# Kernel tuning notes

Measured on AMD Instinct MI355X. Metric: run time of the kernel, lower is better.

## Reference

```python
import jax, jax.numpy as jnp
import numpy as np

N, E, D_IN, D_OUT = 50000, 800000, 32, 64


def setup_inputs() -> dict:
    key = jax.random.key(0)
    k1, k2, k3 = jax.random.split(key, 3)
    x = jax.random.normal(k1, (N, D_IN), dtype=jnp.float32)
    edge_index = jax.random.randint(k2, (2, E), 0, N)
    W = jax.random.normal(k3, (D_IN, D_OUT), dtype=jnp.float32) / np.sqrt(D_IN).astype(np.float32)
    b = jnp.zeros((D_OUT,), dtype=jnp.float32)
    return {"x": x, "edge_index": edge_index, "W": W, "b": b}


def gcn_conv(x, edge_index, W, b):
    n = x.shape[0]
    loop = jnp.arange(n)
    src = jnp.concatenate([edge_index[0], loop])  # message sources (x_j)
    dst = jnp.concatenate([edge_index[1], loop])  # aggregation targets
    xw = x @ W  # [N, D_OUT]
    deg = jax.ops.segment_sum(jnp.ones(src.shape[0], dtype=xw.dtype), dst, num_segments=n)
    dinv = jnp.where(deg > 0, jax.lax.rsqrt(jnp.where(deg > 0, deg, 1.0)), 0.0)
    norm = dinv[src] * dinv[dst]  # [E+N]
    msg = xw[src] * norm[:, None]  # gather + scale
    out = jax.ops.segment_sum(msg, dst, num_segments=n)  # scatter-add aggregate
    return out + b


def reference(x, edge_index, W, b):
    h = jax.nn.relu(gcn_conv(x, edge_index, W, b))
    # InnerProductDecoder over given edges: sigmoid(<h_i, h_j>)
    logits = jnp.sum(h[edge_index[0]] * h[edge_index[1]], axis=-1)  # [E]
    adj_pred = jax.nn.sigmoid(logits) + 1e-15
    return (adj_pred, edge_index)
```

## Files before the change

### kernel.cpp

```cpp
#include <hip/hip_runtime.h>
#include <hip/hip_fp8.h>

#define D_IN 32
#define D_OUT 64
#define NBMAX 800
#define BIN_BLKS 128
#define COPY_BLKS 784
#define CAP 32
#define BCAP 1280

__device__ __forceinline__ unsigned char f2fp8(float f) {
    __hip_fp8_e4m3 v(f);
    return (unsigned char)v.__x;
}
__device__ __forceinline__ float fp82f(unsigned char u) {
    __hip_fp8_e4m3 v;
    v.__x = (__hip_fp8_storage_t)u;
    return (float)v;
}
__device__ __forceinline__ float bf2f(unsigned short u) {
    return __uint_as_float(((unsigned int)u) << 16);
}
__device__ __forceinline__ unsigned short f2bf(float f) {
    unsigned int x = __float_as_uint(f);
    x += 0x7fff + ((x >> 16) & 1);
    return (unsigned short)(x >> 16);
}
__device__ __forceinline__ float dot4fp8(unsigned int ua, unsigned int ub) {
    float s = 0.f;
#pragma unroll
    for (int k = 0; k < 4; ++k) {
        __hip_fp8_e4m3 fa, fb;
        fa.__x = (__hip_fp8_storage_t)(unsigned char)(ua >> (8 * k));
        fb.__x = (__hip_fp8_storage_t)(unsigned char)(ub >> (8 * k));
        s += (float)fa * (float)fb;
    }
    return s;
}

__global__ void __launch_bounds__(256) k_bin(const int* __restrict__ src,
                                             const int* __restrict__ dst,
                                             int* __restrict__ cellcnt,
                                             int* __restrict__ cells,
                                             const int* __restrict__ ei,
                                             float* __restrict__ outE,
                                             const float* __restrict__ x,
                                             const float* __restrict__ W,
                                             unsigned short* __restrict__ xwb,
                                             int N, int E, int NB, int chunk) {
    int t = threadIdx.x;
    if (blockIdx.x >= BIN_BLKS) {
        int cb = blockIdx.x - BIN_BLKS;
        __shared__ float Ws[D_IN * D_OUT];
        __shared__ float xs[64 * D_IN];
        int node0 = cb * 64;
        for (int i = t; i < D_IN * D_OUT; i += 256) Ws[i] = W[i];
        for (int i = t; i < 64 * (D_IN / 4); i += 256) {
            int r = i >> 3, q = i & 7;
            int node = node0 + r;
            float4 v = make_float4(0.f, 0.f, 0.f, 0.f);
            if (node < N) v = *(const float4*)(x + (size_t)node * D_IN + q * 4);
            *(float4*)(xs + r * D_IN + q * 4) = v;
        }
        __syncthreads();
#pragma unroll
        for (int i = 0; i < 16; ++i) {
            int idx = i * 256 + t;
            int ln = idx >> 6, c = idx & 63;
            int node = node0 + ln;
            if (node < N) {
                float s = 0.f;
#pragma unroll
                for (int k = 0; k < D_IN; ++k) s += xs[ln * D_IN + k] * Ws[k * D_OUT + c];
                xwb[(size_t)node * D_OUT + c] = f2bf(s);
            }
        }
        int ct = cb * 256 + t;
        int cstride = COPY_BLKS * 256;
        int n4 = (2 * E) >> 2;
        const int4* ei4 = (const int4*)ei;
        float4* o4 = (float4*)outE;
        for (int i = ct; i < n4; i += cstride) {
            int4 v = ei4[i];
            o4[i] = make_float4((float)v.x, (float)v.y, (float)v.z, (float)v.w);
        }
        for (int i = n4 * 4 + ct; i < 2 * E; i += cstride) outE[i] = (float)ei[i];
        return;
    }
    __shared__ int cur[NBMAX];
    int blk = blockIdx.x;
    int s0 = blk * chunk;
    int s1 = s0 + chunk; if (s1 > E) s1 = E;
    for (int i = t; i < NB; i += 256) cur[i] = 0;
    __syncthreads();
    if (s0 < E) {
        for (int k = s0 + t * 8; k < s1; k += 2048) {
            if (k + 7 < s1) {
                int4 sa = *(const int4*)(src + k);
                int4 sb = *(const int4*)(src + k + 4);
                int4 da = *(const int4*)(dst + k);
                int4 db = *(const int4*)(dst + k + 4);
                int s8[8] = {sa.x, sa.y, sa.z, sa.w, sb.x, sb.y, sb.z, sb.w};
                int d8[8] = {da.x, da.y, da.z, da.w, db.x, db.y, db.z, db.w};
#pragma unroll
                for (int u = 0; u < 8; ++u) {
                    int d = d8[u], bin = d >> 6;
                    int pos = atomicAdd(&cur[bin], 1);
                    if (pos < CAP)
                        cells[((size_t)bin * BIN_BLKS + blk) * CAP + pos] = (s8[u] << 6) | (d & 63);
                }
            } else {
                for (int e = k; e < s1; ++e) {
                    int d = dst[e], bin = d >> 6;
                    int pos = atomicAdd(&cur[bin], 1);
                    if (pos < CAP)
                        cells[((size_t)bin * BIN_BLKS + blk) * CAP + pos] = (src[e] << 6) | (d & 63);
                }
            }
        }
    }
    __syncthreads();
    for (int i = t; i < NB; i += 256) cellcnt[(size_t)blk * NB + i] = min(cur[i], CAP);
}

__global__ void __launch_bounds__(256) k_build(const unsigned short* __restrict__ xwb,
                                               const int* __restrict__ cellcnt,
                                               const int* __restrict__ cells,
                                               float* __restrict__ dinv,
                                               int* __restrict__ offs, int* __restrict__ ends,
                                               int* __restrict__ srcs,
                                               unsigned char* __restrict__ xws, int N, int NB) {
    __shared__ int ebuf[BIN_BLKS * CAP];
    __shared__ int ccnt[BIN_BLKS], coff[BIN_BLKS + 1];
    __shared__ int lcnt[64], lofs[65], lcur[64];
    __shared__ float ds[64];
    int bin = blockIdx.x, t = threadIdx.x;
    int node0 = bin * 64;
    if (t < 64) { lcnt[t] = 0; lcur[t] = 0; }
    if (t < BIN_BLKS) ccnt[t] = cellcnt[(size_t)t * NB + bin];
    __syncthreads();
    if (t == 0) {
        int r = 0;
#pragma unroll
        for (int i = 0; i < BIN_BLKS; ++i) { coff[i] = r; r += ccnt[i]; }
        coff[BIN_BLKS] = r;
    }
    __syncthreads();
    const int* crow = cells + (size_t)bin * BIN_BLKS * CAP;
#pragma unroll
    for (int i = 0; i < (BIN_BLKS * CAP) / 256; ++i) {
        int idx = i * 256 + t;
        int cell = idx >> 5, pos = idx & (CAP - 1);
        if (pos < ccnt[cell]) {
            int p = crow[idx];
            ebuf[coff[cell] + pos] = p;
            atomicAdd(&lcnt[p & 63], 1);
        }
    }
    __syncthreads();
    int ns = coff[BIN_BLKS];
    if (t == 0) {
        int r = 0;
#pragma unroll
        for (int i = 0; i < 64; ++i) { lofs[i] = r; r += lcnt[i]; }
        lofs[64] = r;
    }
    __syncthreads();
    int binbase = bin * BCAP;
    if (t < 64) {
        float d = rsqrtf((float)(lcnt[t] + 1));
        ds[t] = d;
        int node = node0 + t;
        if (node < N) {
            dinv[node] = d;
            offs[node] = binbase + lofs[t];
            ends[node] = binbase + lofs[t + 1];
        }
    }
    __syncthreads();
    for (int k = t; k < ns; k += 256) {
        int p = ebuf[k];
        int d = p & 63;
        int slot = atomicAdd(&lcur[d], 1);
        srcs[binbase + lofs[d] + slot] = p >> 6;
    }
#pragma unroll
    for (int i = 0; i < 16; ++i) {
        int idx = i * 256 + t;
        int ln = idx >> 6, c = idx & 63;
        int node = node0 + ln;
        if (node < N)
            xws[(size_t)node * D_OUT + c] = f2fp8(bf2f(xwb[(size_t)node * D_OUT + c]) * ds[ln]);
    }
}

__global__ void k_agg(const unsigned char* __restrict__ xws, const float* __restrict__ dinv,
                      const int* __restrict__ offs, const int* __restrict__ ends,
                      const int* __restrict__ srcs,
                      const float* __restrict__ b, unsigned char* __restrict__ h, int n) {
    int g = blockIdx.x * blockDim.x + threadIdx.x;
    int d = g >> 6, c = g & 63;
    if (d >= n) return;
    float dd = dinv[d];
    float a0 = fp82f(xws[(size_t)d * D_OUT + c]);
    float a1 = 0.f, a2 = 0.f, a3 = 0.f;
    int kend = ends[d];
    for (int k = offs[d]; k < kend; k += 8) {
        int s[8];
        float v[8];
#pragma unroll
        for (int u = 0; u < 8; ++u) {
            int t = k + u;
            s[u] = srcs[t < kend ? t : kend - 1];
        }
#pragma unroll
        for (int u = 0; u < 8; ++u) {
            float xv = fp82f(xws[(size_t)s[u] * D_OUT + c]);
            v[u] = (k + u < kend) ? xv : 0.f;
        }
        a0 += v[0]; a1 += v[1]; a2 += v[2]; a3 += v[3];
        a0 += v[4]; a1 += v[5]; a2 += v[6]; a3 += v[7];
    }
    float r = dd * ((a0 + a1) + (a2 + a3)) + b[c];
    h[(size_t)d * D_OUT + c] = f2fp8(r > 0.f ? r : 0.f);
}

__global__ void k_decode(const int* __restrict__ e0, const int* __restrict__ e1,
                         const unsigned char* __restrict__ h, float* __restrict__ out,
                         int E, int halfE) {
    int g = blockIdx.x * blockDim.x + threadIdx.x;
    int pair = g >> 1, q = g & 1;
    if (pair >= halfE) return;
    int ea = pair;
    int eb = pair + halfE;
    bool hasB = eb < E;
    int ia = e0[ea], ja = e1[ea];
    int ib = hasB ? e0[eb] : ia;
    int jb = hasB ? e1[eb] : ja;
    const uint4* hia = (const uint4*)(h + (size_t)ia * D_OUT + q * 32);
    const uint4* hja = (const uint4*)(h + (size_t)ja * D_OUT + q * 32);
    const uint4* hib = (const uint4*)(h + (size_t)ib * D_OUT + q * 32);
    const uint4* hjb = (const uint4*)(h + (size_t)jb * D_OUT + q * 32);
    uint4 a0 = hia[0], a1 = hia[1];
    uint4 b0 = hja[0], b1 = hja[1];
    uint4 c0 = hib[0], c1 = hib[1];
    uint4 d0 = hjb[0], d1 = hjb[1];
    float pa = dot4fp8(a0.x, b0.x) + dot4fp8(a0.y, b0.y)
             + dot4fp8(a0.z, b0.z) + dot4fp8(a0.w, b0.w)
             + dot4fp8(a1.x, b1.x) + dot4fp8(a1.y, b1.y)
             + dot4fp8(a1.z, b1.z) + dot4fp8(a1.w, b1.w);
    float pb = dot4fp8(c0.x, d0.x) + dot4fp8(c0.y, d0.y)
             + dot4fp8(c0.z, d0.z) + dot4fp8(c0.w, d0.w)
             + dot4fp8(c1.x, d1.x) + dot4fp8(c1.y, d1.y)
             + dot4fp8(c1.z, d1.z) + dot4fp8(c1.w, d1.w);
    pa += __shfl_xor(pa, 1, 64);
    pb += __shfl_xor(pb, 1, 64);
    if (q == 0) {
        out[ea] = 1.0f / (1.0f + expf(-pa)) + 1e-15f;
        if (hasB) out[eb] = 1.0f / (1.0f + expf(-pb)) + 1e-15f;
    }
}

extern "C" void kernel_launch(void* const* d_in, const int* in_sizes, int n_in,
                              void* d_out, int out_size, void* d_ws, size_t ws_size,
                              hipStream_t stream) {
    const float* x = (const float*)d_in[0];
    const int*   ei = (const int*)d_in[1];
    const float* W = (const float*)d_in[2];
    const float* b = (const float*)d_in[3];

    const int N = in_sizes[0] / D_IN;
    const int E = in_sizes[1] / 2;
    const size_t NF = (size_t)N * D_OUT;
    const int NB = (N + 63) >> 6;

    float* out = (float*)d_out;

    char* base = (char*)d_ws;
    unsigned char*  xws     = (unsigned char*)base;
    unsigned char*  h       = (unsigned char*)(base + NF);
    unsigned short* xwb     = (unsigned short*)(base + NF * 2);
    float*          dinv    = (float*)(base + NF * 4);
    int*            offs    = (int*)(base + NF * 4 + (size_t)N * 4);
    int*            ends    = offs + N;
    int*            cellcnt = ends + N;
    int*            srcs    = cellcnt + (size_t)BIN_BLKS * NB;
    int*            cells   = srcs + (size_t)NB * BCAP;

    const int* srcv = ei;
    const int* dstv = ei + E;

    const int B = 256;
    const int gNF = (int)((NF + B - 1) / B);
    const int halfE = (E + 1) / 2;
    const int gD  = (int)(((long long)halfE * 2 + B - 1) / B);
    const int chunk = ((E + BIN_BLKS - 1) / BIN_BLKS + 7) & ~7;

    k_bin   <<<BIN_BLKS + COPY_BLKS, B, 0, stream>>>(srcv, dstv, cellcnt, cells,
                                                     ei, out + E, x, W, xwb, N, E, NB, chunk);
    k_build <<<NB,  B, 0, stream>>>(xwb, cellcnt, cells, dinv, offs, ends, srcs, xws, N, NB);
    k_agg   <<<gNF, B, 0, stream>>>(xws, dinv, offs, ends, srcs, b, h, N);
    k_decode<<<gD,  B, 0, stream>>>(srcv, dstv, h, out, E, halfE);
}
```

Measured before the change: 78.62 us.

## Store unscaled XW as fp8 and apply source degree scaling during aggregation

The matmul stage now writes XW directly as fp8 instead of bf16, and the build kernel no longer rescales XW by dinv into a second fp8 buffer. The aggregation kernel instead loads dinv[src] per neighbour and multiplies it in. This removes a bf16 write, a bf16 read and an fp8 rewrite of the full N×64 feature matrix, in exchange for an extra random 4-byte gather per edge in the aggregation loop. Quantising before scaling also changes fp8 rounding behaviour.

```diff
diff --git a/kernel.cpp b/kernel.cpp
--- a/kernel.cpp
+++ b/kernel.cpp
@@ -17,14 +17,6 @@
     __hip_fp8_e4m3 v;
     v.__x = (__hip_fp8_storage_t)u;
     return (float)v;
-}
-__device__ __forceinline__ float bf2f(unsigned short u) {
-    return __uint_as_float(((unsigned int)u) << 16);
-}
-__device__ __forceinline__ unsigned short f2bf(float f) {
-    unsigned int x = __float_as_uint(f);
-    x += 0x7fff + ((x >> 16) & 1);
-    return (unsigned short)(x >> 16);
 }
 __device__ __forceinline__ float dot4fp8(unsigned int ua, unsigned int ub) {
     float s = 0.f;
@@ -46,7 +38,7 @@
                                              float* __restrict__ outE,
                                              const float* __restrict__ x,
                                              const float* __restrict__ W,
-                                             unsigned short* __restrict__ xwb,
+                                             unsigned char* __restrict__ xws,
                                              int N, int E, int NB, int chunk) {
     int t = threadIdx.x;
     if (blockIdx.x >= BIN_BLKS) {
@@ -72,7 +64,7 @@
                 float s = 0.f;
 #pragma unroll
                 for (int k = 0; k < D_IN; ++k) s += xs[ln * D_IN + k] * Ws[k * D_OUT + c];
-                xwb[(size_t)node * D_OUT + c] = f2bf(s);
+                xws[(size_t)node * D_OUT + c] = f2fp8(s);
             }
         }
         int ct = cb * 256 + t;
@@ -123,17 +115,15 @@
     for (int i = t; i < NB; i += 256) cellcnt[(size_t)blk * NB + i] = min(cur[i], CAP);
 }
 
-__global__ void __launch_bounds__(256) k_build(const unsigned short* __restrict__ xwb,
-                                               const int* __restrict__ cellcnt,
+__global__ void __launch_bounds__(256) k_build(const int* __restrict__ cellcnt,
                                                const int* __restrict__ cells,
                                                float* __restrict__ dinv,
                                                int* __restrict__ offs, int* __restrict__ ends,
                                                int* __restrict__ srcs,
-                                               unsigned char* __restrict__ xws, int N, int NB) {
+                                               int N, int NB) {
     __shared__ int ebuf[BIN_BLKS * CAP];
     __shared__ int ccnt[BIN_BLKS], coff[BIN_BLKS + 1];
     __shared__ int lcnt[64], lofs[65], lcur[64];
-    __shared__ float ds[64];
     int bin = blockIdx.x, t = threadIdx.x;
     int node0 = bin * 64;
     if (t < 64) { lcnt[t] = 0; lcur[t] = 0; }
@@ -168,11 +158,9 @@
     __syncthreads();
     int binbase = bin * BCAP;
     if (t < 64) {
-        float d = rsqrtf((float)(lcnt[t] + 1));
-        ds[t] = d;
         int node = node0 + t;
         if (node < N) {
-            dinv[node] = d;
+            dinv[node] = rsqrtf((float)(lcnt[t] + 1));
             offs[node] = binbase + lofs[t];
             ends[node] = binbase + lofs[t + 1];
         }
@@ -183,14 +171,6 @@
         int d = p & 63;
         int slot = atomicAdd(&lcur[d], 1);
         srcs[binbase + lofs[d] + slot] = p >> 6;
-    }
-#pragma unroll
-    for (int i = 0; i < 16; ++i) {
-        int idx = i * 256 + t;
-        int ln = idx >> 6, c = idx & 63;
-        int node = node0 + ln;
-        if (node < N)
-            xws[(size_t)node * D_OUT + c] = f2fp8(bf2f(xwb[(size_t)node * D_OUT + c]) * ds[ln]);
     }
 }
 
@@ -202,12 +182,12 @@
     int d = g >> 6, c = g & 63;
     if (d >= n) return;
     float dd = dinv[d];
-    float a0 = fp82f(xws[(size_t)d * D_OUT + c]);
+    float a0 = fp82f(xws[(size_t)d * D_OUT + c]) * dd;
     float a1 = 0.f, a2 = 0.f, a3 = 0.f;
     int kend = ends[d];
     for (int k = offs[d]; k < kend; k += 8) {
         int s[8];
-        float v[8];
+        float v[8], w[8];
 #pragma unroll
         for (int u = 0; u < 8; ++u) {
             int t = k + u;
@@ -216,10 +196,11 @@
 #pragma unroll
         for (int u = 0; u < 8; ++u) {
             float xv = fp82f(xws[(size_t)s[u] * D_OUT + c]);
+            w[u] = dinv[s[u]];
             v[u] = (k + u < kend) ? xv : 0.f;
         }
-        a0 += v[0]; a1 += v[1]; a2 += v[2]; a3 += v[3];
-        a0 += v[4]; a1 += v[5]; a2 += v[6]; a3 += v[7];
+        a0 += v[0] * w[0]; a1 += v[1] * w[1]; a2 += v[2] * w[2]; a3 += v[3] * w[3];
+        a0 += v[4] * w[4]; a1 += v[5] * w[5]; a2 += v[6] * w[6]; a3 += v[7] * w[7];
     }
     float r = dd * ((a0 + a1) + (a2 + a3)) + b[c];
     h[(size_t)d * D_OUT + c] = f2fp8(r > 0.f ? r : 0.f);
@@ -279,9 +260,8 @@
     char* base = (char*)d_ws;
     unsigned char*  xws     = (unsigned char*)base;
     unsigned char*  h       = (unsigned char*)(base + NF);
-    unsigned short* xwb     = (unsigned short*)(base + NF * 2);
-    float*          dinv    = (float*)(base + NF * 4);
-    int*            offs    = (int*)(base + NF * 4 + (size_t)N * 4);
+    float*          dinv    = (float*)(base + NF * 2);
+    int*            offs    = (int*)(base + NF * 2 + (size_t)N * 4);
     int*            ends    = offs + N;
     int*            cellcnt = ends + N;
     int*            srcs    = cellcnt + (size_t)BIN_BLKS * NB;
@@ -297,8 +277,8 @@
     const int chunk = ((E + BIN_BLKS - 1) / BIN_BLKS + 7) & ~7;
 
     k_bin   <<<BIN_BLKS + COPY_BLKS, B, 0, stream>>>(srcv, dstv, cellcnt, cells,
-                                                     ei, out + E, x, W, xwb, N, E, NB, chunk);
-    k_build <<<NB,  B, 0, stream>>>(xwb, cellcnt, cells, dinv, offs, ends, srcs, xws, N, NB);
+                                                     ei, out + E, x, W, xws, N, E, NB, chunk);
+    k_build <<<NB,  B, 0, stream>>>(cellcnt, cells, dinv, offs, ends, srcs, N, NB);
     k_agg   <<<gNF, B, 0, stream>>>(xws, dinv, offs, ends, srcs, b, h, N);
     k_decode<<<gD,  B, 0, stream>>>(srcv, dstv, h, out, E, halfE);
 }
```

Result: faster. 75.53 us (median of 3 runs) (-3.9%).
